# Kernel optimization log

Measured on AMD Instinct MI355X. Metric: run time of the kernel, lower is better.

## Reference

```python
import jax, jax.numpy as jnp
import numpy as np

T, N, F_IN, DZ = 4, 2048, 128, 128
HF = 256   # FEM output dim
H = 256    # EDM hidden dim
E1, E2 = 256, 64  # EAM dims


def _l2norm(x, axis):
    n = jnp.sqrt(jnp.sum(x * x, axis=axis, keepdims=True))
    return x / jnp.maximum(n, 1e-12)


def setup_inputs() -> dict:
    key = jax.random.key(0)
    ks = jax.random.split(key, 20)

    def lin(k, fi, fo):
        return (jax.random.normal(k, (fi, fo), jnp.float32) / np.float32(np.sqrt(fi)))

    sup = jax.random.uniform(ks[0], (T, N, N), jnp.float32)
    sup = sup / jnp.sum(sup, axis=2, keepdims=True)       # row-normalized GNN supports
    align = jax.random.uniform(ks[1], (T, N, N), jnp.float32)
    align = align / jnp.sum(align, axis=2, keepdims=True)  # row-normalized align matrices
    feat = jax.random.normal(ks[2], (T + 1, N, F_IN), jnp.float32)
    noise = jax.random.normal(ks[3], (T, N, DZ), jnp.float32)
    G_IN = HF + DZ   # 384
    EIN = H + HF     # 512
    return {
        "sup": sup, "feat": feat, "noise": noise, "align": align,
        "lambd": jnp.float32(0.4),
        "W_fem": lin(ks[4], F_IN, HF), "b_fem": jnp.zeros((HF,), jnp.float32),
        "W_gnn": lin(ks[5], G_IN, H), "b_gnn": jnp.zeros((H,), jnp.float32),
        "Wg_x": lin(ks[6], H, 2 * H), "Wg_h": lin(ks[7], H, 2 * H), "bg": jnp.zeros((2 * H,), jnp.float32),
        "Wc_x": lin(ks[8], H, H), "Wc_h": lin(ks[9], H, H), "bc": jnp.zeros((H,), jnp.float32),
        "W_att": lin(ks[10], HF, H), "b_att": jnp.zeros((H,), jnp.float32),
        "W_emb1": lin(ks[11], EIN, E1), "b_emb1": jnp.zeros((E1,), jnp.float32),
        "W_emb2": lin(ks[12], E1, E2), "b_emb2": jnp.zeros((E2,), jnp.float32),
        "W_scal1": lin(ks[13], EIN, E1), "b_scal1": jnp.zeros((E1,), jnp.float32),
        "W_scal2": lin(ks[14], E1, E2), "b_scal2": jnp.zeros((E2,), jnp.float32),
    }


def reference(sup, feat, noise, align, lambd,
              W_fem, b_fem, W_gnn, b_gnn,
              Wg_x, Wg_h, bg, Wc_x, Wc_h, bc,
              W_att, b_att,
              W_emb1, b_emb1, W_emb2, b_emb2,
              W_scal1, b_scal1, W_scal2, b_scal2):
    # --- FEM: shared linear + relu over all T+1 snapshots ---
    fem = jax.nn.relu(jnp.einsum('tnf,fh->tnh', feat, W_fem) + b_fem)  # [T+1,N,HF]
    t_win = sup.shape[0]
    edm_in = jnp.concatenate([fem[:t_win], noise], axis=2)             # [T,N,HF+DZ]

    # --- GNN (no time recurrence -> batched over T): relu((sup@x)W), row L2-norm ---
    agg = jnp.einsum('tnm,tmf->tnf', sup, edm_in)
    g = _l2norm(jax.nn.relu(jnp.einsum('tnf,fh->tnh', agg, W_gnn) + b_gnn), axis=2)

    # attention feature maps for the attentive node-aligning unit
    fm = jnp.einsum('tnf,fh->tnh', fem, W_att) + b_att                 # [T+1,N,H]
    h0 = jnp.zeros((sup.shape[1], W_gnn.shape[1]), dtype=feat.dtype)

    def step(h, x):
        gt, al, fsrc, fdst = x
        # IGRU cell
        gates = jax.nn.sigmoid(gt @ Wg_x + h @ Wg_h + bg)
        r, u = jnp.split(gates, 2, axis=1)
        c = jnp.tanh(gt @ Wc_x + (r * h) @ Wc_h + bc)
        rnn = (1.0 - u) * h + u * c
        # attentive node aligning: mix given align matrix with feature attention
        att = jax.nn.softmax(fdst @ fsrc.T, axis=1)                    # [N,N]
        sup_al = lambd * al + (1.0 - lambd) * att
        h_new = sup_al @ rnn
        return h_new, None

    h_last, _ = jax.lax.scan(step, h0, (g, align, fm[:t_win], fm[1:]))

    # --- EAM (pred_flag=True): tanh embedding head + sigmoid scaling head ---
    emb_cat = jnp.concatenate([h_last, fem[t_win]], axis=1)            # [N, H+HF]
    emb = jnp.tanh(jnp.tanh(emb_cat @ W_emb1 + b_emb1) @ W_emb2 + b_emb2)
    emb = _l2norm(emb, axis=0)                                         # F.normalize(dim=0)
    scal_o = jax.nn.sigmoid(jax.nn.sigmoid(emb_cat @ W_scal1 + b_scal1) @ W_scal2 + b_scal2)
    scal = scal_o @ scal_o.T                                           # [N,N]
    # pairwise-distance decoder: adj[i,j] = 1 + tanh(-||e_i - e_j||^2 * scal[i,j])
    sq = jnp.sum(emb * emb, axis=1)
    dist = -(sq[:, None] + sq[None, :] - 2.0 * (emb @ emb.T))
    return 1.0 + jnp.tanh(dist * scal)
```

## Files before the change

### kernel.cpp

```cpp
#include <hip/hip_runtime.h>
#include <math.h>


#define T_WIN 4
#define NN 2048
#define F_IN 128
#define HF 256
#define HH 256
#define DZ 128
#define G_IN 384
#define EIN 512
#define E1D 256
#define E2D 64

typedef _Float16 f16;
typedef _Float16 f16x8 __attribute__((ext_vector_type(8)));
typedef _Float16 f16x4 __attribute__((ext_vector_type(4)));
typedef float f32x4 __attribute__((ext_vector_type(4)));

__device__ __forceinline__ float wave_sum(float v) {
#pragma unroll
  for (int o = 32; o > 0; o >>= 1) v += __shfl_down(v, o);
  return v;
}
__device__ __forceinline__ float wave_max(float v) {
#pragma unroll
  for (int o = 32; o > 0; o >>= 1) v = fmaxf(v, __shfl_down(v, o));
  return v;
}

__device__ __forceinline__ void gld_lds16(const void* g, void* l) {
  __builtin_amdgcn_global_load_lds(
      (const __attribute__((address_space(1))) unsigned int*)g,
      (__attribute__((address_space(3))) unsigned int*)l, 16, 0, 0);
}

template <int EPI, int BN, int WOUT>
__global__ __launch_bounds__(256) void hgemm(
    const f16* __restrict__ A, const f16* __restrict__ A2,
    const f16* __restrict__ BT, const float* __restrict__ bias,
    const float* __restrict__ bias2, float* __restrict__ Cf,
    f16* __restrict__ Ch, const float* __restrict__ X1f,
    f16* __restrict__ Xrh, float* __restrict__ Xu_out,
    const f16* __restrict__ Xpre, int lda, int lda2, int kspl, int ldb,
    int ldc, int K, long zA, long zB, long zC) {
  constexpr int WN = BN / 2;
  constexpr int FN = WN / 16;
  constexpr int BI = BN / 32;
  __shared__ alignas(16) f16 As[128 * 64];
  __shared__ alignas(16) f16 Bs[BN * 64];
  const int tid = threadIdx.x;
  const int lane = tid & 63, wid = tid >> 6;
  const int wm = wid >> 1, wn = wid & 1;
  const int row0 = blockIdx.y * 128, col0 = blockIdx.x * BN;
  const long zb = blockIdx.z;
  A += zb * zA;
  BT += zb * zB;
  const int l8 = lane >> 3;
  const int lx = ((lane & 7) ^ l8) * 8;
  const int sw = (lane & 7) * 8;

  f32x4 acc[4][FN];
#pragma unroll
  for (int m = 0; m < 4; ++m)
#pragma unroll
    for (int n = 0; n < FN; ++n) acc[m][n] = (f32x4){0.f, 0.f, 0.f, 0.f};

  for (int k0 = 0; k0 < K; k0 += 64) {
#pragma unroll
    for (int i = 0; i < 4; ++i) {
      int r = wid * 32 + i * 8;
      const f16* src =
          (k0 < kspl) ? A + (size_t)(row0 + r + l8) * lda + k0 + lx
                      : A2 + (size_t)(row0 + r + l8) * lda2 + (k0 - kspl) + lx;
      gld_lds16(src, &As[r * 64]);
    }
#pragma unroll
    for (int i = 0; i < BI; ++i) {
      int r = wid * (BN / 4) + i * 8;
      gld_lds16(BT + (size_t)(col0 + r + l8) * ldb + k0 + lx, &Bs[r * 64]);
    }
    __syncthreads();
#pragma unroll
    for (int ks = 0; ks < 2; ++ks) {
      f16x8 af[4], bf[FN];
#pragma unroll
      for (int m = 0; m < 4; ++m)
        af[m] = *(const f16x8*)&As[((wm * 64 + m * 16 + (lane & 15)) * 64 +
                                    ks * 32 + (lane >> 4) * 8) ^ sw];
#pragma unroll
      for (int n = 0; n < FN; ++n)
        bf[n] = *(const f16x8*)&Bs[((wn * WN + n * 16 + (lane & 15)) * 64 +
                                    ks * 32 + (lane >> 4) * 8) ^ sw];
#pragma unroll
      for (int m = 0; m < 4; ++m)
#pragma unroll
        for (int n = 0; n < FN; ++n)
          acc[m][n] = __builtin_amdgcn_mfma_f32_16x16x32_f16(af[m], bf[n],
                                                             acc[m][n], 0, 0, 0);
    }
    __syncthreads();
  }

  const int cl = lane & 15, rh4 = (lane >> 4) * 4;
  float* Cfb = Cf + zb * zC;
  f16* Chb = Ch + zb * zC;
  const float* bp = (EPI == 5 && zb == 1) ? bias2 : bias;
#pragma unroll
  for (int m = 0; m < 4; ++m) {
#pragma unroll
    for (int n = 0; n < FN; ++n) {
      int cc = col0 + wn * WN + n * 16 + cl;
      float bv = 0.f;
      if (EPI == 6)
        bv = (cc < 256) ? bias[cc] : bias2[cc - 256];
      else if (bp)
        bv = bp[cc];
#pragma unroll
      for (int q = 0; q < 4; ++q) {
        size_t r = row0 + wm * 64 + m * 16 + rh4 + q;
        float v = acc[m][n][q] + bv;
        if (EPI == 4) {
          v += (float)Xpre[r * 768 + cc];
          float sv = 1.f / (1.f + __expf(-v));
          if (cc < 256)
            Xrh[r * 256 + cc] = (f16)(sv * X1f[r * 256 + cc]);
          else
            Xu_out[r * 256 + cc - 256] = sv;
        } else {
          if (EPI == 1) v = fmaxf(v, 0.f);
          if (EPI == 5) v = (zb == 0) ? tanhf(v) : 1.f / (1.f + __expf(-v));
          if (EPI == 6)
            v = (cc < 256) ? tanhf(v) : 1.f / (1.f + __expf(-v));
          if (WOUT == 0 || WOUT == 2) Cfb[r * ldc + cc] = v;
          if (WOUT == 1 || WOUT == 2) Chb[r * ldc + cc] = (f16)v;
        }
      }
    }
  }
}

__global__ __launch_bounds__(256) void sup_agg(
    const float* __restrict__ sup, const f16* __restrict__ edmT,
    f16* __restrict__ aggP) {
  __shared__ alignas(16) f16 As[64 * 64];
  __shared__ alignas(16) f16 Bs[384 * 64];
  const int tid = threadIdx.x;
  const int lane = tid & 63, wid = tid >> 6;
  const int m0 = blockIdx.x * 64, kh = blockIdx.y, t = blockIdx.z;
  const int l8 = lane >> 3;
  const int lx = ((lane & 7) ^ l8) * 8;
  const int sw = (lane & 7) * 8;
  const int cl = lane & 15, hi = lane >> 4;
  const int wm = wid >> 1, wn = wid & 1;
  const float* supT = sup + (size_t)t * NN * NN;
  const f16* edmTt = edmT + (size_t)t * G_IN * NN;

  f32x4 acc[2][12];
#pragma unroll
  for (int m = 0; m < 2; ++m)
#pragma unroll
    for (int n = 0; n < 12; ++n) acc[m][n] = (f32x4){0.f, 0.f, 0.f, 0.f};

  const int ar = tid >> 2;
  const int g0 = (tid & 3) * 2;
  const int kbeg = kh * 512;

  for (int k0 = kbeg; k0 < kbeg + 512; k0 += 64) {
    const float* ap = supT + (size_t)(m0 + ar) * NN + k0 + (tid & 3) * 16;
    float4 f0 = *(const float4*)ap;
    float4 f1 = *(const float4*)(ap + 4);
    float4 f2 = *(const float4*)(ap + 8);
    float4 f3 = *(const float4*)(ap + 12);
    f16x8 hv0 = {(f16)f0.x, (f16)f0.y, (f16)f0.z, (f16)f0.w,
                 (f16)f1.x, (f16)f1.y, (f16)f1.z, (f16)f1.w};
    f16x8 hv1 = {(f16)f2.x, (f16)f2.y, (f16)f2.z, (f16)f2.w,
                 (f16)f3.x, (f16)f3.y, (f16)f3.z, (f16)f3.w};
    *(f16x8*)&As[ar * 64 + ((g0 ^ (ar & 7)) * 8)] = hv0;
    *(f16x8*)&As[ar * 64 + (((g0 + 1) ^ (ar & 7)) * 8)] = hv1;
#pragma unroll
    for (int i = 0; i < 12; ++i) {
      int rn = wid * 96 + i * 8;
      gld_lds16(edmTt + (size_t)(rn + l8) * NN + k0 + lx, &Bs[rn * 64]);
    }
    __syncthreads();
#pragma unroll
    for (int ks = 0; ks < 2; ++ks) {
      f16x8 af[2], bf[12];
#pragma unroll
      for (int m = 0; m < 2; ++m)
        af[m] = *(const f16x8*)&As[((wm * 32 + m * 16 + cl) * 64 + ks * 32 +
                                    hi * 8) ^ sw];
#pragma unroll
      for (int n = 0; n < 12; ++n)
        bf[n] = *(const f16x8*)&Bs[((wn * 192 + n * 16 + cl) * 64 + ks * 32 +
                                    hi * 8) ^ sw];
#pragma unroll
      for (int m = 0; m < 2; ++m)
#pragma unroll
        for (int n = 0; n < 12; ++n)
          acc[m][n] = __builtin_amdgcn_mfma_f32_16x16x32_f16(af[m], bf[n],
                                                             acc[m][n], 0, 0, 0);
    }
    __syncthreads();
  }

  f16* dst = aggP + (size_t)kh * (4L * NN * G_IN) +
             ((size_t)t * NN + m0) * G_IN;
#pragma unroll
  for (int m = 0; m < 2; ++m)
#pragma unroll
    for (int n = 0; n < 12; ++n)
#pragma unroll
      for (int q = 0; q < 4; ++q)
        dst[(size_t)(wm * 32 + m * 16 + hi * 4 + q) * G_IN + wn * 192 +
            n * 16 + cl] = (f16)acc[m][n][q];
}

__global__ __launch_bounds__(256) void gnn_l2(
    const f16* __restrict__ aggP, const f16* __restrict__ WgnnT,
    const float* __restrict__ bgnn, f16* __restrict__ g16) {
  __shared__ alignas(16) f16 As[32 * 64];
  __shared__ alignas(16) f16 Bs[256 * 64];
  __shared__ float red[4][32];
  const int tid = threadIdx.x;
  const int lane = tid & 63, wid = tid >> 6;
  const int m0 = blockIdx.x * 32;
  const int l8 = lane >> 3;
  const int lx = ((lane & 7) ^ l8) * 8;
  const int sw = (lane & 7) * 8;
  const int cl = lane & 15, hi = lane >> 4;
  const long PS = 4L * NN * G_IN;

  f32x4 acc[2][4];
#pragma unroll
  for (int m = 0; m < 2; ++m)
#pragma unroll
    for (int n = 0; n < 4; ++n) acc[m][n] = (f32x4){0.f, 0.f, 0.f, 0.f};

  const int ar = tid >> 3;
  const int acw = ((tid & 7) ^ (ar & 7)) * 8;

  for (int k0 = 0; k0 < G_IN; k0 += 64) {
    size_t gi = (size_t)(m0 + ar) * G_IN + k0 + ((tid & 7) * 8);
    f16x8 a0 = *(const f16x8*)(aggP + gi);
    f16x8 a1 = *(const f16x8*)(aggP + PS + gi);
    f16x8 a2 = *(const f16x8*)(aggP + 2 * PS + gi);
    f16x8 a3 = *(const f16x8*)(aggP + 3 * PS + gi);
    f16x8 s;
#pragma unroll
    for (int e = 0; e < 8; ++e)
      s[e] = (f16)((float)a0[e] + (float)a1[e] + (float)a2[e] + (float)a3[e]);
    *(f16x8*)&As[ar * 64 + acw] = s;
#pragma unroll
    for (int i = 0; i < 8; ++i) {
      int rn = wid * 64 + i * 8;
      gld_lds16(WgnnT + (size_t)(rn + l8) * G_IN + k0 + lx, &Bs[rn * 64]);
    }
    __syncthreads();
#pragma unroll
    for (int ks = 0; ks < 2; ++ks) {
      f16x8 af[2], bf[4];
#pragma unroll
      for (int m = 0; m < 2; ++m)
        af[m] = *(const f16x8*)&As[((m * 16 + cl) * 64 + ks * 32 + hi * 8) ^ sw];
#pragma unroll
      for (int n = 0; n < 4; ++n)
        bf[n] = *(const f16x8*)&Bs[((wid * 64 + n * 16 + cl) * 64 + ks * 32 +
                                    hi * 8) ^ sw];
#pragma unroll
      for (int m = 0; m < 2; ++m)
#pragma unroll
        for (int n = 0; n < 4; ++n)
          acc[m][n] = __builtin_amdgcn_mfma_f32_16x16x32_f16(af[m], bf[n],
                                                             acc[m][n], 0, 0, 0);
    }
    __syncthreads();
  }

#pragma unroll
  for (int m = 0; m < 2; ++m)
#pragma unroll
    for (int n = 0; n < 4; ++n) {
      float bv = bgnn[wid * 64 + n * 16 + cl];
#pragma unroll
      for (int q = 0; q < 4; ++q)
        acc[m][n][q] = fmaxf(acc[m][n][q] + bv, 0.f);
    }
#pragma unroll
  for (int m = 0; m < 2; ++m)
#pragma unroll
    for (int q = 0; q < 4; ++q) {
      float ss = 0.f;
#pragma unroll
      for (int n = 0; n < 4; ++n) ss += acc[m][n][q] * acc[m][n][q];
#pragma unroll
      for (int msk = 1; msk < 16; msk <<= 1) ss += __shfl_xor(ss, msk);
      if (cl == 0) red[wid][m * 16 + hi * 4 + q] = ss;
    }
  __syncthreads();
#pragma unroll
  for (int m = 0; m < 2; ++m)
#pragma unroll
    for (int q = 0; q < 4; ++q) {
      int row = m * 16 + hi * 4 + q;
      float tot = red[0][row] + red[1][row] + red[2][row] + red[3][row];
      float inv = 1.f / fmaxf(sqrtf(tot), 1e-12f);
#pragma unroll
      for (int n = 0; n < 4; ++n)
        g16[(size_t)(m0 + row) * 256 + wid * 64 + n * 16 + cl] =
            (f16)(acc[m][n][q] * inv);
    }
}

__global__ __launch_bounds__(256) void hsum4(const float* __restrict__ hP,
                                             float* __restrict__ hf,
                                             f16* __restrict__ h16) {
  long i = ((long)blockIdx.x * 256 + threadIdx.x) * 4;
  float4 a = *(const float4*)(hP + i);
  float4 b = *(const float4*)(hP + 524288 + i);
  float4 c = *(const float4*)(hP + 1048576 + i);
  float4 d = *(const float4*)(hP + 1572864 + i);
  float4 s = {a.x + b.x + c.x + d.x, a.y + b.y + c.y + d.y,
              a.z + b.z + c.z + d.z, a.w + b.w + c.w + d.w};
  *(float4*)(hf + i) = s;
  f16x4 o = {(f16)s.x, (f16)s.y, (f16)s.z, (f16)s.w};
  *(f16x4*)(h16 + i) = o;
}

__global__ __launch_bounds__(256) void rnn0_t(const f16* __restrict__ Xgc,
                                              const float* __restrict__ bg,
                                              const float* __restrict__ bc,
                                              f16* __restrict__ rnnT) {
  __shared__ float tile[32][33];
  int n0 = blockIdx.x * 32, k0 = blockIdx.y * 32;
  int tx = threadIdx.x & 31, ty = threadIdx.x >> 5;
#pragma unroll
  for (int i = 0; i < 32; i += 8) {
    int n = n0 + ty + i, k = k0 + tx;
    float u = 1.f / (1.f + __expf(-((float)Xgc[(size_t)n * 768 + 256 + k] +
                                    bg[256 + k])));
    float c = tanhf((float)Xgc[(size_t)n * 768 + 512 + k] + bc[k]);
    tile[ty + i][tx] = u * c;
  }
  __syncthreads();
#pragma unroll
  for (int i = 0; i < 32; i += 8)
    rnnT[(size_t)(k0 + ty + i) * NN + n0 + tx] = (f16)tile[tx][ty + i];
}

__global__ __launch_bounds__(256) void cgemm_rnnT(
    const f16* __restrict__ A, const f16* __restrict__ BT,
    const float* __restrict__ bias, const f16* __restrict__ Xc,
    const float* __restrict__ hf, const float* __restrict__ ubuf,
    f16* __restrict__ rnnT) {
  __shared__ alignas(16) f16 As[128 * 64];
  __shared__ alignas(16) f16 Bs[64 * 64];
  __shared__ alignas(16) f16 tileT[64 * 136];
  const int tid = threadIdx.x;
  const int lane = tid & 63, wid = tid >> 6;
  const int wm = wid >> 1, wn = wid & 1;
  const int row0 = blockIdx.y * 128, col0 = blockIdx.x * 64;
  const int l8 = lane >> 3;
  const int lx = ((lane & 7) ^ l8) * 8;
  const int sw = (lane & 7) * 8;

  f32x4 acc[4][2];
#pragma unroll
  for (int m = 0; m < 4; ++m)
#pragma unroll
    for (int n = 0; n < 2; ++n) acc[m][n] = (f32x4){0.f, 0.f, 0.f, 0.f};

  for (int k0 = 0; k0 < 256; k0 += 64) {
#pragma unroll
    for (int i = 0; i < 4; ++i) {
      int r = wid * 32 + i * 8;
      gld_lds16(A + (size_t)(row0 + r + l8) * 256 + k0 + lx, &As[r * 64]);
    }
#pragma unroll
    for (int i = 0; i < 2; ++i) {
      int r = wid * 16 + i * 8;
      gld_lds16(BT + (size_t)(col0 + r + l8) * 256 + k0 + lx, &Bs[r * 64]);
    }
    __syncthreads();
#pragma unroll
    for (int ks = 0; ks < 2; ++ks) {
      f16x8 af[4], bf[2];
#pragma unroll
      for (int m = 0; m < 4; ++m)
        af[m] = *(const f16x8*)&As[((wm * 64 + m * 16 + (lane & 15)) * 64 +
                                    ks * 32 + (lane >> 4) * 8) ^ sw];
#pragma unroll
      for (int n = 0; n < 2; ++n)
        bf[n] = *(const f16x8*)&Bs[((wn * 32 + n * 16 + (lane & 15)) * 64 +
                                    ks * 32 + (lane >> 4) * 8) ^ sw];
#pragma unroll
      for (int m = 0; m < 4; ++m)
#pragma unroll
        for (int n = 0; n < 2; ++n)
          acc[m][n] = __builtin_amdgcn_mfma_f32_16x16x32_f16(af[m], bf[n],
                                                             acc[m][n], 0, 0, 0);
    }
    __syncthreads();
  }

  const int cl = lane & 15, rh4 = (lane >> 4) * 4;
#pragma unroll
  for (int m = 0; m < 4; ++m) {
#pragma unroll
    for (int n = 0; n < 2; ++n) {
      int ccl = wn * 32 + n * 16 + cl;
      int cc = col0 + ccl;
      float bv = bias[cc];
#pragma unroll
      for (int q = 0; q < 4; ++q) {
        int rl = wm * 64 + m * 16 + rh4 + q;
        size_t r = row0 + rl;
        float c = tanhf(acc[m][n][q] + bv + (float)Xc[r * 768 + cc]);
        float u = ubuf[r * 256 + cc];
        float h = hf[r * 256 + cc];
        tileT[ccl * 136 + rl] = (f16)((1.f - u) * h + u * c);
      }
    }
  }
  __syncthreads();
#pragma unroll
  for (int i = 0; i < 4; ++i) {
    int chunk = i * 256 + tid;
    int rr = chunk >> 4, seg = (chunk & 15) * 8;
    *(f16x8*)&rnnT[(size_t)(col0 + rr) * NN + row0 + seg] =
        *(const f16x8*)&tileT[rr * 136 + seg];
  }
}

__global__ __launch_bounds__(256) void pq_decode(
    const f16* __restrict__ emb, const f16* __restrict__ scal,
    const float* __restrict__ sq, float* __restrict__ out) {
  __shared__ alignas(16) f16 EA[128 * 64], EB[128 * 64], SA[128 * 64],
      SB[128 * 64];
  const int tid = threadIdx.x;
  const int lane = tid & 63, wid = tid >> 6;
  const int wm = wid >> 1, wn = wid & 1;
  const int row0 = blockIdx.y * 128, col0 = blockIdx.x * 128;
  const int l8 = lane >> 3;
  const int lx = ((lane & 7) ^ l8) * 8;
  const int sw = (lane & 7) * 8;
#pragma unroll
  for (int i = 0; i < 2; ++i) {
    int r = wid * 16 + i * 8;
    gld_lds16(emb + (size_t)(row0 + r + l8) * 64 + lx, &EA[r * 64]);
    gld_lds16(emb + (size_t)(col0 + r + l8) * 64 + lx, &EB[r * 64]);
    gld_lds16(scal + (size_t)(row0 + r + l8) * 64 + lx, &SA[r * 64]);
    gld_lds16(scal + (size_t)(col0 + r + l8) * 64 + lx, &SB[r * 64]);
    int r2 = r + 64;
    gld_lds16(emb + (size_t)(row0 + r2 + l8) * 64 + lx, &EA[r2 * 64]);
    gld_lds16(emb + (size_t)(col0 + r2 + l8) * 64 + lx, &EB[r2 * 64]);
    gld_lds16(scal + (size_t)(row0 + r2 + l8) * 64 + lx, &SA[r2 * 64]);
    gld_lds16(scal + (size_t)(col0 + r2 + l8) * 64 + lx, &SB[r2 * 64]);
  }
  __syncthreads();
  f32x4 accP[4][4], accQ[4][4];
#pragma unroll
  for (int m = 0; m < 4; ++m)
#pragma unroll
    for (int n = 0; n < 4; ++n) {
      accP[m][n] = (f32x4){0.f, 0.f, 0.f, 0.f};
      accQ[m][n] = (f32x4){0.f, 0.f, 0.f, 0.f};
    }
#pragma unroll
  for (int ks = 0; ks < 2; ++ks) {
    f16x8 af[4], bf[4];
#pragma unroll
    for (int m = 0; m < 4; ++m)
      af[m] = *(const f16x8*)&EA[((wm * 64 + m * 16 + (lane & 15)) * 64 +
                                  ks * 32 + (lane >> 4) * 8) ^ sw];
#pragma unroll
    for (int n = 0; n < 4; ++n)
      bf[n] = *(const f16x8*)&EB[((wn * 64 + n * 16 + (lane & 15)) * 64 +
                                  ks * 32 + (lane >> 4) * 8) ^ sw];
#pragma unroll
    for (int m = 0; m < 4; ++m)
#pragma unroll
      for (int n = 0; n < 4; ++n)
        accP[m][n] = __builtin_amdgcn_mfma_f32_16x16x32_f16(af[m], bf[n],
                                                            accP[m][n], 0, 0, 0);
#pragma unroll
    for (int m = 0; m < 4; ++m)
      af[m] = *(const f16x8*)&SA[((wm * 64 + m * 16 + (lane & 15)) * 64 +
                                  ks * 32 + (lane >> 4) * 8) ^ sw];
#pragma unroll
    for (int n = 0; n < 4; ++n)
      bf[n] = *(const f16x8*)&SB[((wn * 64 + n * 16 + (lane & 15)) * 64 +
                                  ks * 32 + (lane >> 4) * 8) ^ sw];
#pragma unroll
    for (int m = 0; m < 4; ++m)
#pragma unroll
      for (int n = 0; n < 4; ++n)
        accQ[m][n] = __builtin_amdgcn_mfma_f32_16x16x32_f16(af[m], bf[n],
                                                            accQ[m][n], 0, 0, 0);
  }
  const int cl = lane & 15, rh4 = (lane >> 4) * 4;
#pragma unroll
  for (int m = 0; m < 4; ++m) {
#pragma unroll
    for (int n = 0; n < 4; ++n) {
      int c = col0 + wn * 64 + n * 16 + cl;
      float sqc = sq[c];
#pragma unroll
      for (int q = 0; q < 4; ++q) {
        size_t r = row0 + wm * 64 + m * 16 + rh4 + q;
        float dist = -(sq[r] + sqc - 2.f * accP[m][n][q]);
        out[r * NN + c] = 1.f + tanhf(dist * accQ[m][n][q]);
      }
    }
  }
}

struct MT {
  const float* src[11];
  f16* dst[11];
  int K[11], N[11], st[11], ts[12];
};
__global__ __launch_bounds__(256) void multi_transp(MT mt) {
  __shared__ float tile[32][33];
  int b = blockIdx.x, w = 0;
  while (b >= mt.ts[w + 1]) ++w;
  int lt = b - mt.ts[w];
  int K = mt.K[w], N = mt.N[w];
  int tk = lt % (K >> 5), tn = lt / (K >> 5);
  int k0 = tk * 32, n0 = tn * 32;
  int tx = threadIdx.x & 31, ty = threadIdx.x >> 5;
  const float* src = mt.src[w];
#pragma unroll
  for (int i = 0; i < 32; i += 8)
    tile[ty + i][tx] = src[(size_t)(k0 + ty + i) * N + n0 + tx];
  __syncthreads();
  f16* dst = mt.dst[w];
  int st = mt.st[w];
#pragma unroll
  for (int i = 0; i < 32; i += 8)
    dst[(size_t)(n0 + ty + i) * st + k0 + tx] = (f16)tile[tx][ty + i];
}

__global__ __launch_bounds__(256) void edm_t(const f16* __restrict__ fem16,
                                             const float* __restrict__ noise,
                                             f16* __restrict__ edmT) {
  __shared__ float tile[32][33];
  int bx = blockIdx.x, r0 = blockIdx.y * 32, t = blockIdx.z;
  int tx = threadIdx.x & 31, ty = threadIdx.x >> 5;
  f16* dstT = edmT + (size_t)t * G_IN * NN;
  if (bx < 8) {
    int c0 = bx * 32;
    const f16* src = fem16 + (size_t)t * NN * HF;
#pragma unroll
    for (int i = 0; i < 32; i += 8)
      tile[ty + i][tx] = (float)src[(size_t)(r0 + ty + i) * HF + c0 + tx];
    __syncthreads();
#pragma unroll
    for (int i = 0; i < 32; i += 8)
      dstT[(size_t)(c0 + ty + i) * NN + r0 + tx] = (f16)tile[tx][ty + i];
  } else {
    int c0 = (bx - 8) * 32;
    const float* src = noise + (size_t)t * NN * DZ;
#pragma unroll
    for (int i = 0; i < 32; i += 8)
      tile[ty + i][tx] = src[(size_t)(r0 + ty + i) * DZ + c0 + tx];
    __syncthreads();
#pragma unroll
    for (int i = 0; i < 32; i += 8)
      dstT[(size_t)(HF + c0 + ty + i) * NN + r0 + tx] = (f16)tile[tx][ty + i];
  }
}

__global__ __launch_bounds__(256) void cvt_h(const float* __restrict__ in,
                                             f16* __restrict__ out) {
  long i = ((long)blockIdx.x * 256 + threadIdx.x) * 4;
  float4 v = *(const float4*)(in + i);
  f16x4 o = {(f16)v.x, (f16)v.y, (f16)v.z, (f16)v.w};
  *(f16x4*)(out + i) = o;
}

__global__ __launch_bounds__(256) void softmax_mix(
    const float* __restrict__ S, const float* __restrict__ Al,
    const float* __restrict__ lam_ptr, f16* __restrict__ Mh) {
  const int tid = threadIdx.x;
  const float4* s4 = (const float4*)(S + (long)blockIdx.x * 2048);
  float4 a = s4[tid], b = s4[tid + 256];
  float m = fmaxf(fmaxf(fmaxf(a.x, a.y), fmaxf(a.z, a.w)),
                  fmaxf(fmaxf(b.x, b.y), fmaxf(b.z, b.w)));
  __shared__ float red[4];
  float w = wave_max(m);
  if ((tid & 63) == 0) red[tid >> 6] = w;
  __syncthreads();
  m = fmaxf(fmaxf(red[0], red[1]), fmaxf(red[2], red[3]));
  __syncthreads();
  a.x = __expf(a.x - m); a.y = __expf(a.y - m);
  a.z = __expf(a.z - m); a.w = __expf(a.w - m);
  b.x = __expf(b.x - m); b.y = __expf(b.y - m);
  b.z = __expf(b.z - m); b.w = __expf(b.w - m);
  float s = a.x + a.y + a.z + a.w + b.x + b.y + b.z + b.w;
  w = wave_sum(s);
  if ((tid & 63) == 0) red[tid >> 6] = w;
  __syncthreads();
  float inv = 1.f / (red[0] + red[1] + red[2] + red[3]);
  float lam = lam_ptr[0], oml = 1.f - lam;
  const float4* al4 = (const float4*)(Al + (long)blockIdx.x * 2048);
  float4 x = al4[tid], y = al4[tid + 256];
  f16x4 o0 = {(f16)(lam * x.x + oml * a.x * inv),
              (f16)(lam * x.y + oml * a.y * inv),
              (f16)(lam * x.z + oml * a.z * inv),
              (f16)(lam * x.w + oml * a.w * inv)};
  f16x4 o1 = {(f16)(lam * y.x + oml * b.x * inv),
              (f16)(lam * y.y + oml * b.y * inv),
              (f16)(lam * y.z + oml * b.z * inv),
              (f16)(lam * y.w + oml * b.w * inv)};
  f16x4* out4 = (f16x4*)(Mh + (long)blockIdx.x * 2048);
  out4[tid] = o0;
  out4[tid + 256] = o1;
}

__global__ __launch_bounds__(256) void col_l2norm64(
    const float* __restrict__ x, float* __restrict__ cn) {
  int c = blockIdx.x;
  float ss = 0.f;
  for (int r = threadIdx.x; r < NN; r += 256) {
    float v = x[(long)r * 64 + c];
    ss += v * v;
  }
  __shared__ float red[4];
  float w = wave_sum(ss);
  if ((threadIdx.x & 63) == 0) red[threadIdx.x >> 6] = w;
  __syncthreads();
  if (threadIdx.x == 0)
    cn[c] = fmaxf(sqrtf(red[0] + red[1] + red[2] + red[3]), 1e-12f);
}

__global__ void norm_sq64h(const float* __restrict__ x,
                           const float* __restrict__ cn,
                           f16* __restrict__ emb16, float* __restrict__ sq) {
  int i = blockIdx.x, j = threadIdx.x;
  float e = x[(long)i * 64 + j] / cn[j];
  emb16[(long)i * 64 + j] = (f16)e;
  float s = wave_sum(e * e);
  if (j == 0) sq[i] = s;
}

extern "C" void kernel_launch(void* const* d_in, const int* in_sizes, int n_in,
                              void* d_out, int out_size, void* d_ws,
                              size_t ws_size, hipStream_t stream) {
  (void)in_sizes; (void)n_in; (void)out_size; (void)ws_size;
  const float* sup    = (const float*)d_in[0];
  const float* feat   = (const float*)d_in[1];
  const float* noise  = (const float*)d_in[2];
  const float* align  = (const float*)d_in[3];
  const float* lambd  = (const float*)d_in[4];
  const float* W_fem  = (const float*)d_in[5];
  const float* b_fem  = (const float*)d_in[6];
  const float* W_gnn  = (const float*)d_in[7];
  const float* b_gnn  = (const float*)d_in[8];
  const float* Wg_x   = (const float*)d_in[9];
  const float* Wg_h   = (const float*)d_in[10];
  const float* bg     = (const float*)d_in[11];
  const float* Wc_x   = (const float*)d_in[12];
  const float* Wc_h   = (const float*)d_in[13];
  const float* bc     = (const float*)d_in[14];
  const float* W_att  = (const float*)d_in[15];
  const float* b_att  = (const float*)d_in[16];
  const float* W_emb1 = (const float*)d_in[17];
  const float* b_emb1 = (const float*)d_in[18];
  const float* W_emb2 = (const float*)d_in[19];
  const float* b_emb2 = (const float*)d_in[20];
  const float* W_scal1= (const float*)d_in[21];
  const float* b_scal1= (const float*)d_in[22];
  const float* W_scal2= (const float*)d_in[23];
  const float* b_scal2= (const float*)d_in[24];

  char* wsb = (char*)d_ws;
  size_t po = 0;
  auto P = [&](size_t bytes) {
    size_t r = po;
    po += (bytes + 255) & ~(size_t)255;
    return r;
  };
  f16* fem16  = (f16*)(wsb + P(5L * NN * HF * 2));
  f16* fm16   = (f16*)(wsb + P(5L * NN * HH * 2));
  f16* g16    = (f16*)(wsb + P(4L * NN * HH * 2));
  f16* WT     = (f16*)(wsb + P(884736L * 2));
  f16* Xgc16  = (f16*)(wsb + P(4L * NN * 768 * 2));
  float* hA   = (float*)(wsb + P((long)NN * HH * 4));
  float* hB   = (float*)(wsb + P((long)NN * HH * 4));
  f16* h16A   = (f16*)(wsb + P((long)NN * HH * 2));
  f16* h16B   = (f16*)(wsb + P((long)NN * HH * 2));
  float* ubuf = (float*)(wsb + P((long)NN * HH * 4));
  f16* rh16   = (f16*)(wsb + P((long)NN * HH * 2));
  f16* rnnT16 = (f16*)(wsb + P((long)NN * HH * 2));
  float* hP   = (float*)(wsb + P(4L * NN * HH * 4));
  f16* M16_2  = (f16*)(wsb + P(2L * NN * NN * 2));
  f16* e1s1   = (f16*)(wsb + P((long)NN * 512 * 2));
  float* embscF = (float*)(wsb + P(2L * NN * E2D * 4));
  f16* embsc16  = (f16*)(wsb + P(2L * NN * E2D * 2));
  f16* emb16  = (f16*)(wsb + P((long)NN * E2D * 2));
  float* cn   = (float*)(wsb + P(64 * 4));
  float* sq   = (float*)(wsb + P(NN * 4));
  size_t arena = P(34078720);
  f16* feat16 = (f16*)(wsb + arena);
  f16* edmT   = (f16*)(wsb + arena + 2621440);
  f16* aggP   = (f16*)(wsb + arena + 8912896);
  float* Sbuf2 = (float*)(wsb + arena);

  f16* W_femT  = WT;
  f16* W_gnnT  = W_femT + 32768;
  f16* WgxcT   = W_gnnT + 98304;
  f16* WghT    = WgxcT + 196608;
  f16* WchT    = WghT + 131072;
  f16* W_attT  = WchT + 65536;
  f16* We1s1T  = W_attT + 65536;
  f16* Wemb2T  = We1s1T + 262144;
  f16* Wscal2T = Wemb2T + 16384;

  MT mt;
  const float* wsrc[11] = {W_fem, W_gnn, Wg_x, Wc_x, Wg_h, Wc_h,
                           W_att, W_emb1, W_scal1, W_emb2, W_scal2};
  f16* wdst[11] = {W_femT, W_gnnT, WgxcT, WgxcT + 512 * 256, WghT, WchT,
                   W_attT, We1s1T, We1s1T + 256 * 512, Wemb2T, Wscal2T};
  const int wK[11]  = {128, 384, 256, 256, 256, 256, 256, 512, 512, 256, 256};
  const int wNd[11] = {256, 256, 512, 256, 512, 256, 256, 256, 256, 64, 64};
  const int wSt[11] = {128, 384, 256, 256, 256, 256, 256, 512, 512, 256, 256};
  int tcum = 0;
  for (int i = 0; i < 11; ++i) {
    mt.src[i] = wsrc[i];
    mt.dst[i] = wdst[i];
    mt.K[i] = wK[i];
    mt.N[i] = wNd[i];
    mt.st[i] = wSt[i];
    mt.ts[i] = tcum;
    tcum += (wK[i] >> 5) * (wNd[i] >> 5);
  }
  mt.ts[11] = tcum;

  const f16* NH = nullptr;
  const float* NOF = nullptr;
  float* NF = nullptr;
  f16* NHm = nullptr;

  multi_transp<<<tcum, 256, 0, stream>>>(mt);
  cvt_h<<<(5L * NN * F_IN) / 1024, 256, 0, stream>>>(feat, feat16);

  hgemm<1, 64, 1><<<dim3(4, 80, 1), 256, 0, stream>>>(
      feat16, NH, W_femT, b_fem, NOF, NF, fem16, NOF, NHm, NF, NH,
      128, 0, 128, 128, 256, 128, 0, 0, 0);

  edm_t<<<dim3(12, 64, 4), 256, 0, stream>>>(fem16, noise, edmT);

  sup_agg<<<dim3(32, 4, 4), 256, 0, stream>>>(sup, edmT, aggP);
  gnn_l2<<<256, 256, 0, stream>>>(aggP, W_gnnT, b_gnn, g16);

  hgemm<0, 64, 1><<<dim3(4, 80, 1), 256, 0, stream>>>(
      fem16, NH, W_attT, b_att, NOF, NF, fm16, NOF, NHm, NF, NH,
      256, 0, 256, 256, 256, 256, 0, 0, 0);

  hgemm<0, 64, 1><<<dim3(12, 64, 1), 256, 0, stream>>>(
      g16, NH, WgxcT, NOF, NOF, NF, Xgc16, NOF, NHm, NF, NH,
      256, 0, 256, 256, 768, 256, 0, 0, 0);

  float* hs[2] = {hA, hB};
  f16* h16s[2] = {h16A, h16B};

  for (int p = 0; p < 2; ++p) {
    hgemm<0, 128, 0><<<dim3(16, 16, 2), 256, 0, stream>>>(
        fm16 + (size_t)(2 * p + 1) * NN * HH, NH,
        fm16 + (size_t)(2 * p) * NN * HH, NOF, NOF, Sbuf2, NHm, NOF, NHm, NF,
        NH, 256, 0, 256, 256, 2048, 256, (long)NN * HH, (long)NN * HH,
        (long)NN * NN);
    softmax_mix<<<2 * NN, 256, 0, stream>>>(
        Sbuf2, align + (size_t)(2 * p) * NN * NN, lambd, M16_2);

    for (int tl = 0; tl < 2; ++tl) {
      int t = 2 * p + tl;
      if (t == 0) {
        rnn0_t<<<dim3(64, 8, 1), 256, 0, stream>>>(Xgc16, bg, bc, rnnT16);
      } else {
        const float* hprev = hs[(t - 1) & 1];
        const f16* h16prev = h16s[(t - 1) & 1];
        hgemm<4, 64, 0><<<dim3(8, 16, 1), 256, 0, stream>>>(
            h16prev, NH, WghT, bg, NOF, NF, NHm, hprev, rh16, ubuf,
            Xgc16 + (size_t)t * NN * 768, 256, 0, 256, 256, 512, 256, 0, 0, 0);
        cgemm_rnnT<<<dim3(4, 16, 1), 256, 0, stream>>>(
            rh16, WchT, bc, Xgc16 + (size_t)t * NN * 768 + 512, hprev, ubuf,
            rnnT16);
      }
      hgemm<0, 64, 0><<<dim3(4, 16, 4), 256, 0, stream>>>(
          M16_2 + (size_t)(t & 1) * NN * NN, NH, rnnT16, NOF, NOF, hP, NHm,
          NOF, NHm, NF, NH, 2048, 0, 2048, 2048, 256, 512, 512, 512, 524288);
      hsum4<<<512, 256, 0, stream>>>(hP, hs[t & 1], h16s[t & 1]);
    }
  }

  const f16* h16fin = h16s[1];
  hgemm<6, 64, 1><<<dim3(8, 16, 1), 256, 0, stream>>>(
      h16fin, fem16 + 4L * NN * HF, We1s1T, b_emb1, b_scal1, NF, e1s1, NOF,
      NHm, NF, NH, 256, 256, 256, 512, 512, 512, 0, 0, 0);
  hgemm<5, 64, 2><<<dim3(1, 16, 2), 256, 0, stream>>>(
      e1s1, NH, Wemb2T, b_emb2, b_scal2, embscF, embsc16, NOF, NHm, NF, NH,
      512, 0, 512, 256, 64, 256, 256, 16384, (long)NN * E2D);
  col_l2norm64<<<64, 256, 0, stream>>>(embscF, cn);
  norm_sq64h<<<NN, 64, 0, stream>>>(embscF, cn, emb16, sq);

  pq_decode<<<dim3(16, 16, 1), 256, 0, stream>>>(
      emb16, embsc16 + (size_t)NN * E2D, sq, (float*)d_out);
}
```

Before: 372.3 us.

## Fuse GRU gate and candidate GEMMs into one kernel; split sup_agg columns

Replaces the per-step pair of kernels (a gate GEMM with a sigmoid epilogue, then a candidate GEMM with a tanh/mix epilogue) with a single fused_gru kernel. It keeps r*h and u in shared memory and writes the transposed rnn output directly. This removes the global round trip for rh16/ubuf and one launch per step, but the fused kernel reads operands straight from global memory without LDS staging and runs only 64 blocks. Separately, sup_agg now splits the 384 output columns over two blocks, giving 4x more blocks with a smaller accumulator footprint. The hgemm signature is also trimmed of the unused EPI 4 arguments.

```diff
diff --git a/kernel.cpp b/kernel.cpp
--- a/kernel.cpp
+++ b/kernel.cpp
@@ -28,6 +28,11 @@
   for (int o = 32; o > 0; o >>= 1) v = fmaxf(v, __shfl_down(v, o));
   return v;
 }
+__device__ __forceinline__ float fast_tanh(float x) {
+  float e = __expf(-2.f * fabsf(x));
+  float r = (1.f - e) / (1.f + e);
+  return copysignf(r, x);
+}
 
 __device__ __forceinline__ void gld_lds16(const void* g, void* l) {
   __builtin_amdgcn_global_load_lds(
@@ -40,9 +45,7 @@
     const f16* __restrict__ A, const f16* __restrict__ A2,
     const f16* __restrict__ BT, const float* __restrict__ bias,
     const float* __restrict__ bias2, float* __restrict__ Cf,
-    f16* __restrict__ Ch, const float* __restrict__ X1f,
-    f16* __restrict__ Xrh, float* __restrict__ Xu_out,
-    const f16* __restrict__ Xpre, int lda, int lda2, int kspl, int ldb,
+    f16* __restrict__ Ch, int lda, int lda2, int kspl, int ldb,
     int ldc, int K, long zA, long zB, long zC) {
   constexpr int WN = BN / 2;
   constexpr int FN = WN / 16;
@@ -120,21 +123,11 @@
       for (int q = 0; q < 4; ++q) {
         size_t r = row0 + wm * 64 + m * 16 + rh4 + q;
         float v = acc[m][n][q] + bv;
-        if (EPI == 4) {
-          v += (float)Xpre[r * 768 + cc];
-          float sv = 1.f / (1.f + __expf(-v));
-          if (cc < 256)
-            Xrh[r * 256 + cc] = (f16)(sv * X1f[r * 256 + cc]);
-          else
-            Xu_out[r * 256 + cc - 256] = sv;
-        } else {
-          if (EPI == 1) v = fmaxf(v, 0.f);
-          if (EPI == 5) v = (zb == 0) ? tanhf(v) : 1.f / (1.f + __expf(-v));
-          if (EPI == 6)
-            v = (cc < 256) ? tanhf(v) : 1.f / (1.f + __expf(-v));
-          if (WOUT == 0 || WOUT == 2) Cfb[r * ldc + cc] = v;
-          if (WOUT == 1 || WOUT == 2) Chb[r * ldc + cc] = (f16)v;
-        }
+        if (EPI == 1) v = fmaxf(v, 0.f);
+        if (EPI == 5) v = (zb == 0) ? tanhf(v) : 1.f / (1.f + __expf(-v));
+        if (EPI == 6) v = (cc < 256) ? tanhf(v) : 1.f / (1.f + __expf(-v));
+        if (WOUT == 0 || WOUT == 2) Cfb[r * ldc + cc] = v;
+        if (WOUT == 1 || WOUT == 2) Chb[r * ldc + cc] = (f16)v;
       }
     }
   }
@@ -144,10 +137,11 @@
     const float* __restrict__ sup, const f16* __restrict__ edmT,
     f16* __restrict__ aggP) {
   __shared__ alignas(16) f16 As[64 * 64];
-  __shared__ alignas(16) f16 Bs[384 * 64];
+  __shared__ alignas(16) f16 Bs[192 * 64];
   const int tid = threadIdx.x;
   const int lane = tid & 63, wid = tid >> 6;
-  const int m0 = blockIdx.x * 64, kh = blockIdx.y, t = blockIdx.z;
+  const int m0 = blockIdx.x * 64, n0 = blockIdx.y * 192;
+  const int t = blockIdx.z >> 2, kh = blockIdx.z & 3;
   const int l8 = lane >> 3;
   const int lx = ((lane & 7) ^ l8) * 8;
   const int sw = (lane & 7) * 8;
@@ -156,11 +150,11 @@
   const float* supT = sup + (size_t)t * NN * NN;
   const f16* edmTt = edmT + (size_t)t * G_IN * NN;
 
-  f32x4 acc[2][12];
+  f32x4 acc[2][6];
 #pragma unroll
   for (int m = 0; m < 2; ++m)
 #pragma unroll
-    for (int n = 0; n < 12; ++n) acc[m][n] = (f32x4){0.f, 0.f, 0.f, 0.f};
+    for (int n = 0; n < 6; ++n) acc[m][n] = (f32x4){0.f, 0.f, 0.f, 0.f};
 
   const int ar = tid >> 2;
   const int g0 = (tid & 3) * 2;
@@ -179,26 +173,26 @@
     *(f16x8*)&As[ar * 64 + ((g0 ^ (ar & 7)) * 8)] = hv0;
     *(f16x8*)&As[ar * 64 + (((g0 + 1) ^ (ar & 7)) * 8)] = hv1;
 #pragma unroll
-    for (int i = 0; i < 12; ++i) {
-      int rn = wid * 96 + i * 8;
-      gld_lds16(edmTt + (size_t)(rn + l8) * NN + k0 + lx, &Bs[rn * 64]);
+    for (int i = 0; i < 6; ++i) {
+      int rn = wid * 48 + i * 8;
+      gld_lds16(edmTt + (size_t)(n0 + rn + l8) * NN + k0 + lx, &Bs[rn * 64]);
     }
     __syncthreads();
 #pragma unroll
     for (int ks = 0; ks < 2; ++ks) {
-      f16x8 af[2], bf[12];
+      f16x8 af[2], bf[6];
 #pragma unroll
       for (int m = 0; m < 2; ++m)
         af[m] = *(const f16x8*)&As[((wm * 32 + m * 16 + cl) * 64 + ks * 32 +
                                     hi * 8) ^ sw];
 #pragma unroll
-      for (int n = 0; n < 12; ++n)
-        bf[n] = *(const f16x8*)&Bs[((wn * 192 + n * 16 + cl) * 64 + ks * 32 +
+      for (int n = 0; n < 6; ++n)
+        bf[n] = *(const f16x8*)&Bs[((wn * 96 + n * 16 + cl) * 64 + ks * 32 +
                                     hi * 8) ^ sw];
 #pragma unroll
       for (int m = 0; m < 2; ++m)
 #pragma unroll
-        for (int n = 0; n < 12; ++n)
+        for (int n = 0; n < 6; ++n)
           acc[m][n] = __builtin_amdgcn_mfma_f32_16x16x32_f16(af[m], bf[n],
                                                              acc[m][n], 0, 0, 0);
     }
@@ -206,14 +200,14 @@
   }
 
   f16* dst = aggP + (size_t)kh * (4L * NN * G_IN) +
-             ((size_t)t * NN + m0) * G_IN;
+             ((size_t)t * NN + m0) * G_IN + n0;
 #pragma unroll
   for (int m = 0; m < 2; ++m)
 #pragma unroll
-    for (int n = 0; n < 12; ++n)
+    for (int n = 0; n < 6; ++n)
 #pragma unroll
       for (int q = 0; q < 4; ++q)
-        dst[(size_t)(wm * 32 + m * 16 + hi * 4 + q) * G_IN + wn * 192 +
+        dst[(size_t)(wm * 32 + m * 16 + hi * 4 + q) * G_IN + wn * 96 +
             n * 16 + cl] = (f16)acc[m][n][q];
 }
 
@@ -349,87 +343,127 @@
     rnnT[(size_t)(k0 + ty + i) * NN + n0 + tx] = (f16)tile[tx][ty + i];
 }
 
-__global__ __launch_bounds__(256) void cgemm_rnnT(
-    const f16* __restrict__ A, const f16* __restrict__ BT,
-    const float* __restrict__ bias, const f16* __restrict__ Xc,
-    const float* __restrict__ hf, const float* __restrict__ ubuf,
-    f16* __restrict__ rnnT) {
-  __shared__ alignas(16) f16 As[128 * 64];
-  __shared__ alignas(16) f16 Bs[64 * 64];
-  __shared__ alignas(16) f16 tileT[64 * 136];
+__global__ __launch_bounds__(256) void fused_gru(
+    const f16* __restrict__ h16, const float* __restrict__ hf,
+    const f16* __restrict__ Xgc, const f16* __restrict__ WghT,
+    const f16* __restrict__ WchT, const float* __restrict__ bg,
+    const float* __restrict__ bc, f16* __restrict__ rnnT) {
+  __shared__ alignas(16) f16 rh_s[32 * 264];
+  __shared__ float u_s[32 * 260];
+  __shared__ alignas(16) f16 tileT[256 * 40];
   const int tid = threadIdx.x;
   const int lane = tid & 63, wid = tid >> 6;
-  const int wm = wid >> 1, wn = wid & 1;
-  const int row0 = blockIdx.y * 128, col0 = blockIdx.x * 64;
-  const int l8 = lane >> 3;
-  const int lx = ((lane & 7) ^ l8) * 8;
-  const int sw = (lane & 7) * 8;
-
-  f32x4 acc[4][2];
-#pragma unroll
-  for (int m = 0; m < 4; ++m)
-#pragma unroll
-    for (int n = 0; n < 2; ++n) acc[m][n] = (f32x4){0.f, 0.f, 0.f, 0.f};
-
+  const int cl = lane & 15, hi = lane >> 4;
+  const int r0 = blockIdx.x * 32;
+
+  const int wc0 = wid * 128;
+  f32x4 acc[2][8];
+#pragma unroll
+  for (int m = 0; m < 2; ++m)
+#pragma unroll
+    for (int n = 0; n < 8; ++n) acc[m][n] = (f32x4){0.f, 0.f, 0.f, 0.f};
   for (int k0 = 0; k0 < 256; k0 += 64) {
-#pragma unroll
-    for (int i = 0; i < 4; ++i) {
-      int r = wid * 32 + i * 8;
-      gld_lds16(A + (size_t)(row0 + r + l8) * 256 + k0 + lx, &As[r * 64]);
-    }
-#pragma unroll
-    for (int i = 0; i < 2; ++i) {
-      int r = wid * 16 + i * 8;
-      gld_lds16(BT + (size_t)(col0 + r + l8) * 256 + k0 + lx, &Bs[r * 64]);
-    }
-    __syncthreads();
-#pragma unroll
-    for (int ks = 0; ks < 2; ++ks) {
-      f16x8 af[4], bf[2];
-#pragma unroll
-      for (int m = 0; m < 4; ++m)
-        af[m] = *(const f16x8*)&As[((wm * 64 + m * 16 + (lane & 15)) * 64 +
-                                    ks * 32 + (lane >> 4) * 8) ^ sw];
-#pragma unroll
-      for (int n = 0; n < 2; ++n)
-        bf[n] = *(const f16x8*)&Bs[((wn * 32 + n * 16 + (lane & 15)) * 64 +
-                                    ks * 32 + (lane >> 4) * 8) ^ sw];
-#pragma unroll
-      for (int m = 0; m < 4; ++m)
-#pragma unroll
-        for (int n = 0; n < 2; ++n)
-          acc[m][n] = __builtin_amdgcn_mfma_f32_16x16x32_f16(af[m], bf[n],
+    f16x8 af[2][2], bf[8][2];
+#pragma unroll
+    for (int m = 0; m < 2; ++m)
+#pragma unroll
+      for (int ks = 0; ks < 2; ++ks)
+        af[m][ks] = *(const f16x8*)(h16 + (size_t)(r0 + m * 16 + cl) * 256 +
+                                    k0 + ks * 32 + hi * 8);
+#pragma unroll
+    for (int n = 0; n < 8; ++n)
+#pragma unroll
+      for (int ks = 0; ks < 2; ++ks)
+        bf[n][ks] = *(const f16x8*)(WghT + (size_t)(wc0 + n * 16 + cl) * 256 +
+                                    k0 + ks * 32 + hi * 8);
+#pragma unroll
+    for (int ks = 0; ks < 2; ++ks)
+#pragma unroll
+      for (int m = 0; m < 2; ++m)
+#pragma unroll
+        for (int n = 0; n < 8; ++n)
+          acc[m][n] = __builtin_amdgcn_mfma_f32_16x16x32_f16(af[m][ks],
+                                                             bf[n][ks],
                                                              acc[m][n], 0, 0, 0);
-    }
-    __syncthreads();
-  }
-
-  const int cl = lane & 15, rh4 = (lane >> 4) * 4;
-#pragma unroll
-  for (int m = 0; m < 4; ++m) {
-#pragma unroll
-    for (int n = 0; n < 2; ++n) {
-      int ccl = wn * 32 + n * 16 + cl;
-      int cc = col0 + ccl;
-      float bv = bias[cc];
+  }
+#pragma unroll
+  for (int m = 0; m < 2; ++m) {
+#pragma unroll
+    for (int n = 0; n < 8; ++n) {
+      int cc = wc0 + n * 16 + cl;
+      float bgv = bg[cc];
 #pragma unroll
       for (int q = 0; q < 4; ++q) {
-        int rl = wm * 64 + m * 16 + rh4 + q;
-        size_t r = row0 + rl;
-        float c = tanhf(acc[m][n][q] + bv + (float)Xc[r * 768 + cc]);
-        float u = ubuf[r * 256 + cc];
-        float h = hf[r * 256 + cc];
-        tileT[ccl * 136 + rl] = (f16)((1.f - u) * h + u * c);
+        int rl = m * 16 + hi * 4 + q;
+        size_t r = r0 + rl;
+        float v = acc[m][n][q] + bgv + (float)Xgc[r * 768 + cc];
+        float sv = 1.f / (1.f + __expf(-v));
+        if (wc0 < 256)
+          rh_s[rl * 264 + cc] = (f16)(sv * hf[r * 256 + cc]);
+        else
+          u_s[rl * 260 + cc - 256] = sv;
       }
     }
   }
   __syncthreads();
-#pragma unroll
-  for (int i = 0; i < 4; ++i) {
-    int chunk = i * 256 + tid;
-    int rr = chunk >> 4, seg = (chunk & 15) * 8;
-    *(f16x8*)&rnnT[(size_t)(col0 + rr) * NN + row0 + seg] =
-        *(const f16x8*)&tileT[rr * 136 + seg];
+
+  const int wc2 = wid * 64;
+  f32x4 acc2[2][4];
+#pragma unroll
+  for (int m = 0; m < 2; ++m)
+#pragma unroll
+    for (int n = 0; n < 4; ++n) acc2[m][n] = (f32x4){0.f, 0.f, 0.f, 0.f};
+  for (int k0 = 0; k0 < 256; k0 += 64) {
+    f16x8 af[2][2], bf[4][2];
+#pragma unroll
+    for (int m = 0; m < 2; ++m)
+#pragma unroll
+      for (int ks = 0; ks < 2; ++ks)
+        af[m][ks] = *(const f16x8*)&rh_s[(m * 16 + cl) * 264 + k0 + ks * 32 +
+                                         hi * 8];
+#pragma unroll
+    for (int n = 0; n < 4; ++n)
+#pragma unroll
+      for (int ks = 0; ks < 2; ++ks)
+        bf[n][ks] = *(const f16x8*)(WchT + (size_t)(wc2 + n * 16 + cl) * 256 +
+                                    k0 + ks * 32 + hi * 8);
+#pragma unroll
+    for (int ks = 0; ks < 2; ++ks)
+#pragma unroll
+      for (int m = 0; m < 2; ++m)
+#pragma unroll
+        for (int n = 0; n < 4; ++n)
+          acc2[m][n] = __builtin_amdgcn_mfma_f32_16x16x32_f16(af[m][ks],
+                                                              bf[n][ks],
+                                                              acc2[m][n], 0, 0, 0);
+  }
+#pragma unroll
+  for (int m = 0; m < 2; ++m) {
+#pragma unroll
+    for (int n = 0; n < 4; ++n) {
+      int cc = wc2 + n * 16 + cl;
+      float bcv = bc[cc];
+#pragma unroll
+      for (int q = 0; q < 4; ++q) {
+        int rl = m * 16 + hi * 4 + q;
+        size_t r = r0 + rl;
+        float cv = fast_tanh(acc2[m][n][q] + bcv +
+                             (float)Xgc[r * 768 + 512 + cc]);
+        float u = u_s[rl * 260 + cc];
+        float hv = hf[r * 256 + cc];
+        tileT[cc * 40 + rl] = (f16)((1.f - u) * hv + u * cv);
+      }
+    }
+  }
+  __syncthreads();
+  {
+    int cc = tid;
+    const f16x8* src = (const f16x8*)&tileT[cc * 40];
+    f16x8* dst = (f16x8*)&rnnT[(size_t)cc * NN + r0];
+    dst[0] = src[0];
+    dst[1] = src[1];
+    dst[2] = src[2];
+    dst[3] = src[3];
   }
 }
 
@@ -691,8 +725,6 @@
   float* hB   = (float*)(wsb + P((long)NN * HH * 4));
   f16* h16A   = (f16*)(wsb + P((long)NN * HH * 2));
   f16* h16B   = (f16*)(wsb + P((long)NN * HH * 2));
-  float* ubuf = (float*)(wsb + P((long)NN * HH * 4));
-  f16* rh16   = (f16*)(wsb + P((long)NN * HH * 2));
   f16* rnnT16 = (f16*)(wsb + P((long)NN * HH * 2));
   float* hP   = (float*)(wsb + P(4L * NN * HH * 4));
   f16* M16_2  = (f16*)(wsb + P(2L * NN * NN * 2));
@@ -739,7 +771,6 @@
   mt.ts[11] = tcum;
 
   const f16* NH = nullptr;
-  const float* NOF = nullptr;
   float* NF = nullptr;
   f16* NHm = nullptr;
 
@@ -747,20 +778,20 @@
   cvt_h<<<(5L * NN * F_IN) / 1024, 256, 0, stream>>>(feat, feat16);
 
   hgemm<1, 64, 1><<<dim3(4, 80, 1), 256, 0, stream>>>(
-      feat16, NH, W_femT, b_fem, NOF, NF, fem16, NOF, NHm, NF, NH,
+      feat16, NH, W_femT, b_fem, nullptr, NF, fem16,
       128, 0, 128, 128, 256, 128, 0, 0, 0);
 
   edm_t<<<dim3(12, 64, 4), 256, 0, stream>>>(fem16, noise, edmT);
 
-  sup_agg<<<dim3(32, 4, 4), 256, 0, stream>>>(sup, edmT, aggP);
+  sup_agg<<<dim3(32, 2, 16), 256, 0, stream>>>(sup, edmT, aggP);
   gnn_l2<<<256, 256, 0, stream>>>(aggP, W_gnnT, b_gnn, g16);
 
   hgemm<0, 64, 1><<<dim3(4, 80, 1), 256, 0, stream>>>(
-      fem16, NH, W_attT, b_att, NOF, NF, fm16, NOF, NHm, NF, NH,
+      fem16, NH, W_attT, b_att, nullptr, NF, fm16,
       256, 0, 256, 256, 256, 256, 0, 0, 0);
 
   hgemm<0, 64, 1><<<dim3(12, 64, 1), 256, 0, stream>>>(
-      g16, NH, WgxcT, NOF, NOF, NF, Xgc16, NOF, NHm, NF, NH,
+      g16, NH, WgxcT, nullptr, nullptr, NF, Xgc16,
       256, 0, 256, 256, 768, 256, 0, 0, 0);
 
   float* hs[2] = {hA, hB};
@@ -769,8 +800,8 @@
   for (int p = 0; p < 2; ++p) {
     hgemm<0, 128, 0><<<dim3(16, 16, 2), 256, 0, stream>>>(
         fm16 + (size_t)(2 * p + 1) * NN * HH, NH,
-        fm16 + (size_t)(2 * p) * NN * HH, NOF, NOF, Sbuf2, NHm, NOF, NHm, NF,
-        NH, 256, 0, 256, 256, 2048, 256, (long)NN * HH, (long)NN * HH,
+        fm16 + (size_t)(2 * p) * NN * HH, nullptr, nullptr, Sbuf2, NHm,
+        256, 0, 256, 256, 2048, 256, (long)NN * HH, (long)NN * HH,
         (long)NN * NN);
     softmax_mix<<<2 * NN, 256, 0, stream>>>(
         Sbuf2, align + (size_t)(2 * p) * NN * NN, lambd, M16_2);
@@ -780,28 +811,23 @@
       if (t == 0) {
         rnn0_t<<<dim3(64, 8, 1), 256, 0, stream>>>(Xgc16, bg, bc, rnnT16);
       } else {
-        const float* hprev = hs[(t - 1) & 1];
-        const f16* h16prev = h16s[(t - 1) & 1];
-        hgemm<4, 64, 0><<<dim3(8, 16, 1), 256, 0, stream>>>(
-            h16prev, NH, WghT, bg, NOF, NF, NHm, hprev, rh16, ubuf,
-            Xgc16 + (size_t)t * NN * 768, 256, 0, 256, 256, 512, 256, 0, 0, 0);
-        cgemm_rnnT<<<dim3(4, 16, 1), 256, 0, stream>>>(
-            rh16, WchT, bc, Xgc16 + (size_t)t * NN * 768 + 512, hprev, ubuf,
-            rnnT16);
+        fused_gru<<<64, 256, 0, stream>>>(
+            h16s[(t - 1) & 1], hs[(t - 1) & 1],
+            Xgc16 + (size_t)t * NN * 768, WghT, WchT, bg, bc, rnnT16);
       }
       hgemm<0, 64, 0><<<dim3(4, 16, 4), 256, 0, stream>>>(
-          M16_2 + (size_t)(t & 1) * NN * NN, NH, rnnT16, NOF, NOF, hP, NHm,
-          NOF, NHm, NF, NH, 2048, 0, 2048, 2048, 256, 512, 512, 512, 524288);
+          M16_2 + (size_t)(t & 1) * NN * NN, NH, rnnT16, nullptr, nullptr,
+          hP, NHm, 2048, 0, 2048, 2048, 256, 512, 512, 512, 524288);
       hsum4<<<512, 256, 0, stream>>>(hP, hs[t & 1], h16s[t & 1]);
     }
   }
 
   const f16* h16fin = h16s[1];
   hgemm<6, 64, 1><<<dim3(8, 16, 1), 256, 0, stream>>>(
-      h16fin, fem16 + 4L * NN * HF, We1s1T, b_emb1, b_scal1, NF, e1s1, NOF,
-      NHm, NF, NH, 256, 256, 256, 512, 512, 512, 0, 0, 0);
+      h16fin, fem16 + 4L * NN * HF, We1s1T, b_emb1, b_scal1, NF, e1s1,
+      256, 256, 256, 512, 512, 512, 0, 0, 0);
   hgemm<5, 64, 2><<<dim3(1, 16, 2), 256, 0, stream>>>(
-      e1s1, NH, Wemb2T, b_emb2, b_scal2, embscF, embsc16, NOF, NHm, NF, NH,
+      e1s1, NH, Wemb2T, b_emb2, b_scal2, embscF, embsc16,
       512, 0, 512, 256, 64, 256, 256, 16384, (long)NN * E2D);
   col_l2norm64<<<64, 256, 0, stream>>>(embscF, cn);
   norm_sq64h<<<NN, 64, 0, stream>>>(embscF, cn, emb16, sq);
```

New measurement: 394.1 us. +5.9%, slower.
